# Optimization experiments

Hardware: AMD Instinct MI355X
Metric: run time of the kernel (lower is better)

The kernel has to match this reference:

```python
import jax, jax.numpy as jnp
import numpy as np

N_NODES = 200000
N_EDGES = 3200000
N_FEAT = 8
DT_INIT = 0.3
DT_MIN, DT_MAX = 0.02, 2.0
CG_MAX_ITER = 30
CG_TOL = 1e-4
G_INIT = 9.81


def setup_inputs() -> dict:
    key = jax.random.key(0)
    k1, k2, k3, k4 = jax.random.split(key, 4)
    u_now = jax.random.normal(k1, (N_NODES, N_FEAT), dtype=jnp.float32)
    # DAG edges: src < dst (required by the module's topo-level build)
    a = jax.random.randint(k2, (N_EDGES,), 0, N_NODES)
    b = jax.random.randint(k3, (N_EDGES,), 0, N_NODES)
    src = jnp.minimum(a, b)
    dst = jnp.maximum(a, b)
    dst = jnp.where(src == dst, jnp.minimum(dst + 1, N_NODES - 1), dst)
    src = jnp.where(src == dst, jnp.maximum(src - 1, 0), src)
    edge_index = jnp.stack([src, dst]).astype(jnp.int64)
    # edge_attr[:,0]=dx (positive), edge_attr[:,1]=dz
    edge_attr = jax.random.uniform(k4, (N_EDGES, 2), dtype=jnp.float32,
                                   minval=0.05, maxval=1.0)
    dt = jnp.asarray(DT_INIT, dtype=jnp.float32)
    g_hat = jnp.asarray(G_INIT, dtype=jnp.float32)
    return {"u_now": u_now, "edge_index": edge_index, "edge_attr": edge_attr,
            "dt": dt, "g_hat": g_hat}


def _cg_solve(mv, rhs, max_iter, tol):
    # matches torch cg_solve with x0=None (zeros)
    x = jnp.zeros_like(rhs)
    r = rhs - mv(x)
    p = r
    rs = jnp.sum(r * r)

    def body(i, state):
        x, r, p, rs, done = state
        Ap = mv(p)
        alpha = rs / (jnp.sum(p * Ap) + 1e-12)
        x1 = x + alpha * p
        r1 = r - alpha * Ap
        rs1 = jnp.sum(r1 * r1)
        done1 = done | (jnp.sqrt(rs1) <= tol)
        beta = rs1 / (rs + 1e-12)
        p1 = r1 + beta * p
        sel = lambda old, new: jnp.where(done, old, new)
        return (sel(x, x1), sel(r, r1), sel(p, p1),
                jnp.where(done, rs, rs1), done1)

    x, _, _, _, _ = jax.lax.fori_loop(
        0, max_iter, body, (x, r, p, rs, jnp.array(False)))
    return x


def reference(u_now, edge_index, edge_attr, dt, g_hat):
    src, dst = edge_index[0], edge_index[1]
    E = src.shape[0]
    F = u_now.shape[1]
    dx = jnp.clip(edge_attr[:, 0], 1e-6, None)        # [E]
    inv = (1.0 / dx)[:, None]                         # [E,1]
    slope_e = (edge_attr[:, 1] / dx)[:, None]         # [E,1] dz/dx
    dt_eff = jnp.clip(dt, DT_MIN, DT_MAX)

    def D1(x):  # upwind: out[i] += (x[i]-x[j])*inv_dx
        return jnp.zeros_like(x).at[dst].add((x[dst] - x[src]) * inv)

    def D1_T(y):
        yd = y[dst] * inv
        return jnp.zeros_like(y).at[dst].add(yd).at[src].add(-yd)

    A_mv = lambda v: v + dt_eff * (u_now * D1(v))
    AT_mv = lambda y: y + dt_eff * D1_T(u_now * y)

    # slope source term scattered to dst nodes
    slope_n = jnp.zeros_like(u_now).at[dst].add(
        jnp.broadcast_to(slope_e, (E, F)))
    b = u_now - dt_eff * g_hat * slope_n

    # necg: solve (A^T A) x = A^T b via CG
    rhs = AT_mv(b)
    mv = lambda v: AT_mv(A_mv(v))
    u_next = _cg_solve(mv, rhs, CG_MAX_ITER, CG_TOL)
    return u_next
```

## Files before the change

### kernel.cpp

```cpp
#include <hip/hip_runtime.h>
#include <math.h>
#include <stdint.h>
#include <string.h>


#define F 8
#define CG_ITERS 30
#define LEAF_T 4096
#define LEAF_PAD (LEAF_T + LEAF_T / 128 + 8)
#define ENC_ADD 1024
#define MAX_LEAF 1024
#define MAX_CLS 32


#define LV(A_, i_) A_[(i_) + ((i_) >> 7)]

struct Sched {
    int NL, uNT, uMaxD, nCls;
    int leafOff[MAX_LEAF], leafN[MAX_LEAF], cls[MAX_LEAF];
    int cNB[MAX_CLS], cMaxD[MAX_CLS];
    int cBOff[MAX_CLS][64], cBN[MAX_CLS][64];
    int cA[MAX_CLS][64], cB[MAX_CLS][64], cOrder[MAX_CLS][64];
    int cLevOff[MAX_CLS][32];
    int uA[MAX_LEAF], uB[MAX_LEAF], uOrder[MAX_LEAF], uLevOff[64];
};


static void host_build_tree(int n, int T, int* bOff, int* bN,
                            int* A, int* B, int* dep,
                            int* pNB, int* pNT, int* pMaxD) {
    int so[64], sn[64], st[64], sid[64], sdp[64];
    int sp = 0, coff = 0, cn = n, c2 = 0, t = 0, rootd = 0;
    for (;;) {
        if (cn <= T) {
            if (bOff) { bOff[c2] = coff; bN[c2] = cn; }
            int id = c2, dp = 0; c2++;
            bool fin = false;
            for (;;) {
                if (sp == 0) { rootd = dp; fin = true; break; }
                if (st[sp - 1] == 0) {
                    st[sp - 1] = 1; sid[sp - 1] = id; sdp[sp - 1] = dp;
                    int n2 = sn[sp - 1] / 2; n2 -= (n2 & 7);
                    coff = so[sp - 1] + n2; cn = sn[sp - 1] - n2;
                    break;
                } else {
                    A[t] = sid[sp - 1]; B[t] = id;
                    int dA = sdp[sp - 1];
                    dp = ((dA > dp) ? dA : dp) + 1;
                    dep[t] = dp;
                    id = ENC_ADD + t; t++;
                    sp--;
                }
            }
            if (fin) break;
        } else {
            so[sp] = coff; sn[sp] = cn; st[sp] = 0; sp++;
            int n2 = cn / 2; n2 -= (n2 & 7);
            cn = n2;
        }
    }
    *pNB = c2; *pNT = t; *pMaxD = rootd;
}

static void host_bucketize(const int* dep, int NT, int maxD,
                           int* order, int* levOff) {
    int cnt[64];
    for (int d = 0; d <= maxD; ++d) cnt[d] = 0;
    for (int t = 0; t < NT; ++t) cnt[dep[t]]++;
    int run = 0;
    levOff[0] = 0;
    for (int d = 1; d <= maxD; ++d) { run += cnt[d]; levOff[d] = run; }
    int cur[64];
    for (int d = 1; d <= maxD; ++d) cur[d] = levOff[d - 1];
    for (int t = 0; t < NT; ++t) { int d = dep[t]; order[cur[d]++] = t; }
}

static void build_sched_host(int n, Sched* s) {
    static int uDep[MAX_LEAF];
    host_build_tree(n, LEAF_T, s->leafOff, s->leafN, s->uA, s->uB, uDep,
                    &s->NL, &s->uNT, &s->uMaxD);
    host_bucketize(uDep, s->uNT, s->uMaxD, s->uOrder, s->uLevOff);
    s->nCls = 0;
    int clsN[MAX_CLS];
    int dep[64];
    for (int j = 0; j < s->NL; ++j) {
        int c = -1;
        for (int k = 0; k < s->nCls; ++k)
            if (clsN[k] == s->leafN[j]) { c = k; break; }
        if (c < 0 && s->nCls < MAX_CLS) {
            c = s->nCls++;
            clsN[c] = s->leafN[j];
            int NB, NT, maxD;
            host_build_tree(s->leafN[j], 128, s->cBOff[c], s->cBN[c],
                            s->cA[c], s->cB[c], dep, &NB, &NT, &maxD);
            s->cNB[c] = NB; s->cMaxD[c] = maxD;
            host_bucketize(dep, NT, maxD, s->cOrder[c], s->cLevOff[c]);
        }
        s->cls[j] = c;
    }
}


__device__ __forceinline__ float dt_eff_of(const float* dtp) {
    return fminf(fmaxf(dtp[0], 0.02f), 2.0f);
}

__device__ __forceinline__ int slotOf(int e, int NB) {
    return (e < ENC_ADD) ? e : (NB + (e - ENC_ADD));
}

__device__ __forceinline__ float combine_upper(const float* __restrict__ partial,
                                               const Sched* __restrict__ sc,
                                               float* sU, int lane) {
    int NL = sc->NL, NT = sc->uNT, maxD = sc->uMaxD;
    for (int k = lane; k < NL; k += 256) sU[k] = partial[k];
    __syncthreads();
    for (int d = 1; d <= maxD; ++d) {
        int s0 = sc->uLevOff[d - 1], s1 = sc->uLevOff[d];
        for (int s = s0 + lane; s < s1; s += 256) {
            int tt = sc->uOrder[s];
            sU[NL + tt] = __fadd_rn(sU[slotOf(sc->uA[tt], NL)],
                                    sU[slotOf(sc->uB[tt], NL)]);
        }
        __syncthreads();
    }
    return (NT > 0) ? sU[NL + NT - 1] : sU[0];
}

__device__ __forceinline__ void dot_eval(const float* sA, const float* sB,
                                         float* sChain, float* sVal,
                                         int lane, int NB,
                                         const int* __restrict__ bOff,
                                         const int* __restrict__ bN,
                                         const int* __restrict__ A,
                                         const int* __restrict__ Bb,
                                         const int* __restrict__ order,
                                         const int* __restrict__ levOff,
                                         int maxD,
                                         float* __restrict__ partial, int j) {
    int bb = lane >> 3, jj = lane & 7;
    if (bb < NB) {
        int off = bOff[bb], n = bN[bb];
        if (n >= 8) {
            int lim = n - (n & 7);
            float rr = __fmul_rn(LV(sA, off + jj), LV(sB, off + jj));
            for (int e = jj + 8; e < lim; e += 8)
                rr = __fadd_rn(rr, __fmul_rn(LV(sA, off + e), LV(sB, off + e)));
            sChain[bb * 8 + jj] = rr;
        }
    }
    __syncthreads();
    if (lane < NB) {
        int off = bOff[lane], n = bN[lane];
        float res;
        if (n < 8) {
            res = 0.f;
            for (int e = 0; e < n; ++e)
                res = __fadd_rn(res, __fmul_rn(LV(sA, off + e), LV(sB, off + e)));
        } else {
            int lim = n - (n & 7);
            const float* c = sChain + lane * 8;
            res = __fadd_rn(__fadd_rn(__fadd_rn(c[0], c[1]), __fadd_rn(c[2], c[3])),
                            __fadd_rn(__fadd_rn(c[4], c[5]), __fadd_rn(c[6], c[7])));
            for (int e = lim; e < n; ++e)
                res = __fadd_rn(res, __fmul_rn(LV(sA, off + e), LV(sB, off + e)));
        }
        sVal[lane] = res;
    }
    __syncthreads();
    for (int d = 1; d <= maxD; ++d) {
        int s0 = levOff[d - 1], s1 = levOff[d];
        for (int s = s0 + lane; s < s1; s += 256) {
            int tt = order[s];
            sVal[NB + tt] = __fadd_rn(sVal[slotOf(A[tt], NB)],
                                      sVal[slotOf(Bb[tt], NB)]);
        }
        __syncthreads();
    }
    if (lane == 0) partial[j] = (NB > 1) ? sVal[NB + NB - 2] : sVal[0];
}

__global__ void k_dot_leaf(const float* __restrict__ a, const float* __restrict__ b,
                           const Sched* __restrict__ sc, float* __restrict__ partial) {
    __shared__ float sA[LEAF_PAD], sB[LEAF_PAD];
    __shared__ float sChain[512];
    __shared__ float sVal[160];
    int j = blockIdx.x, lane = threadIdx.x;
    int P = sc->leafOff[j] + 1, nn = sc->leafN[j];
    for (int g = lane; g < nn; g += 256) {
        float av = a[P + g], bv = b[P + g];
        int m = g + (g >> 7);
        sA[m] = av; sB[m] = bv;
    }
    __syncthreads();
    int c = sc->cls[j];
    dot_eval(sA, sB, sChain, sVal, lane, sc->cNB[c], sc->cBOff[c], sc->cBN[c],
             sc->cA[c], sc->cB[c], sc->cOrder[c], sc->cLevOff[c], sc->cMaxD[c],
             partial, j);
}

__global__ void k_dot_rs0(const float* __restrict__ a,
                          const float* __restrict__ partial,
                          const Sched* __restrict__ sc, float* __restrict__ scal) {
    __shared__ float sU[2048];
    int lane = threadIdx.x;
    float res = combine_upper(partial, sc, sU, lane);
    if (lane == 0)
        scal[8 + 0] = __fadd_rn(__fmul_rn(a[0], a[0]), res);
}

__global__ void k_xr_dot(float* __restrict__ x, float* __restrict__ r,
                         const float* __restrict__ p, const float* __restrict__ z,
                         const float* __restrict__ scal,
                         const Sched* __restrict__ sc,
                         const float* __restrict__ partial1,
                         float* __restrict__ partial2, int it) {
    __shared__ float sA[LEAF_PAD];
    __shared__ float sU[2048];
    __shared__ float sChain[512];
    __shared__ float sVal[160];
    __shared__ float sAl;
    __shared__ int   sAct;
    int j = blockIdx.x, lane = threadIdx.x;
    float res = combine_upper(partial1, sc, sU, lane);
    if (lane == 0) {
        float pt = __fadd_rn(__fmul_rn(p[0], z[0]), res);
        sAl = __fdiv_rn(scal[8 + it], __fadd_rn(pt, (float)1e-12));
        sAct = (scal[64 + it] == 0.f) ? 1 : 0;
    }
    __syncthreads();
    int active = sAct;
    float al = sAl;
    int P = sc->leafOff[j] + 1, nn = sc->leafN[j];
    if (j == 0 && lane == 0 && active) {
        x[0] = __fadd_rn(x[0], __fmul_rn(al, p[0]));
        r[0] = __fsub_rn(r[0], __fmul_rn(al, z[0]));
    }
    for (int g = lane; g < nn; g += 256) {
        int q = P + g;
        float rv = r[q];
        if (active) {
            float xv = x[q], pv = p[q], zv = z[q];
            x[q] = __fadd_rn(xv, __fmul_rn(al, pv));
            rv = __fsub_rn(rv, __fmul_rn(al, zv));
            r[q] = rv;
        }
        sA[g + (g >> 7)] = rv;
    }
    __syncthreads();
    int c = sc->cls[j];
    dot_eval(sA, sA, sChain, sVal, lane, sc->cNB[c], sc->cBOff[c], sc->cBN[c],
             sc->cA[c], sc->cB[c], sc->cOrder[c], sc->cLevOff[c], sc->cMaxD[c],
             partial2, j);
}

__global__ void k_p_fin(float4* __restrict__ p4, const float4* __restrict__ r4,
                        const float* __restrict__ rfull,
                        float* __restrict__ scal,
                        const Sched* __restrict__ sc,
                        const float* __restrict__ partial2, int it, int n4) {
    __shared__ float sU[2048];
    __shared__ float sBe;
    __shared__ int   sAct;
    int lane = threadIdx.x;
    float res = combine_upper(partial2, sc, sU, lane);
    if (lane == 0) {
        float rs1 = __fadd_rn(__fmul_rn(rfull[0], rfull[0]), res);
        float RS = scal[8 + it];
        float dn = scal[64 + it];
        sBe = __fdiv_rn(rs1, __fadd_rn(RS, (float)1e-12));
        sAct = (dn == 0.f) ? 1 : 0;
        if (blockIdx.x == 0) {
            scal[8 + it + 1]  = (dn == 0.f) ? rs1 : RS;
            scal[64 + it + 1] = (dn != 0.f || __fsqrt_rn(rs1) <= (float)1e-4)
                                ? 1.f : 0.f;
        }
    }
    __syncthreads();
    if (!sAct) return;
    float be = sBe;
    int i = blockIdx.x * blockDim.x + lane;
    if (i >= n4) return;
    float4 pv = p4[i], rv = r4[i];
    pv.x = __fadd_rn(rv.x, __fmul_rn(be, pv.x));
    pv.y = __fadd_rn(rv.y, __fmul_rn(be, pv.y));
    pv.z = __fadd_rn(rv.z, __fmul_rn(be, pv.z));
    pv.w = __fadd_rn(rv.w, __fmul_rn(be, pv.w));
    p4[i] = pv;
}


__global__ void k_edge_pre(const int* __restrict__ dst, const int* __restrict__ src,
                           int* __restrict__ dstCnt, int* __restrict__ srcCnt, int E) {
    int e = blockIdx.x * blockDim.x + threadIdx.x;
    if (e >= E) return;
    atomicAdd(&dstCnt[dst[e]], 1);
    atomicAdd(&srcCnt[src[e]], 1);
}

__global__ void k_scan1(const int* __restrict__ cnt, int* __restrict__ incl,
                        int* __restrict__ bsums, int N) {
    __shared__ int sm[512];
    int i = blockIdx.x * 512 + threadIdx.x;
    sm[threadIdx.x] = (i < N) ? cnt[i] : 0;
    __syncthreads();
    for (int off = 1; off < 512; off <<= 1) {
        int t = (threadIdx.x >= off) ? sm[threadIdx.x - off] : 0;
        __syncthreads();
        sm[threadIdx.x] += t;
        __syncthreads();
    }
    if (i < N) incl[i] = sm[threadIdx.x];
    if (threadIdx.x == 511) bsums[blockIdx.x] = sm[511];
}

__global__ void k_scan2(int* __restrict__ bsums, int nb) {
    __shared__ int sm[512];
    sm[threadIdx.x] = (threadIdx.x < nb) ? bsums[threadIdx.x] : 0;
    __syncthreads();
    for (int off = 1; off < 512; off <<= 1) {
        int t = (threadIdx.x >= off) ? sm[threadIdx.x - off] : 0;
        __syncthreads();
        sm[threadIdx.x] += t;
        __syncthreads();
    }
    if (threadIdx.x < nb) bsums[threadIdx.x] = sm[threadIdx.x];
}

__global__ void k_scan3(int* __restrict__ off, const int* __restrict__ bsums,
                        const int* __restrict__ cnt, int N, int E) {
    int i = blockIdx.x * 512 + threadIdx.x;
    if (i < N) {
        int add = (blockIdx.x > 0) ? bsums[blockIdx.x - 1] : 0;
        off[i] = off[i] + add - cnt[i];
    }
    if (i == 0) off[N] = E;
}

__global__ void k_fill(const int* __restrict__ dst, const int* __restrict__ src,
                       const int* __restrict__ dstOff, const int* __restrict__ srcOff,
                       int* __restrict__ cursD, int* __restrict__ cursS,
                       int* __restrict__ dstList, int* __restrict__ srcList, int E) {
    int e = blockIdx.x * blockDim.x + threadIdx.x;
    if (e >= E) return;
    int d = dst[e];
    dstList[dstOff[d] + atomicAdd(&cursD[d], 1)] = e;
    int s0 = src[e];
    srcList[srcOff[s0] + atomicAdd(&cursS[s0], 1)] = e;
}

__device__ __forceinline__ void insort(int* L, int lo, int hi) {
    for (int a = lo + 1; a < hi; ++a) {
        int key = L[a]; int b = a - 1;
        while (b >= lo && L[b] > key) { L[b + 1] = L[b]; b--; }
        L[b + 1] = key;
    }
}

__global__ void k_sort(const int* __restrict__ dstOff, const int* __restrict__ srcOff,
                       int* __restrict__ dstList, int* __restrict__ srcList, int N) {
    int i = blockIdx.x * blockDim.x + threadIdx.x;
    if (i >= N) return;
    insort(dstList, dstOff[i], dstOff[i + 1]);
    insort(srcList, srcOff[i], srcOff[i + 1]);
}

__global__ void k_perm(int* dstList, int* srcList,
                       const int* __restrict__ srcp, const int* __restrict__ dstp,
                       const float* __restrict__ ea,
                       float* __restrict__ invD, float* __restrict__ slopeD,
                       float* __restrict__ invS, int E) {
    int k = blockIdx.x * blockDim.x + threadIdx.x;
    if (k >= E) return;
    int e  = dstList[k];
    int e2 = srcList[k];
    float dx  = fmaxf(ea[2 * e], 1e-6f);
    float dx2 = fmaxf(ea[2 * e2], 1e-6f);
    int sA_ = srcp[e];
    int dB_ = dstp[e2];
    float iD = __fdiv_rn(1.f, dx);
    float sD = __fdiv_rn(ea[2 * e + 1], dx);
    float iS = __fdiv_rn(1.f, dx2);
    dstList[k] = sA_;
    srcList[k] = dB_;
    invD[k] = iD; slopeD[k] = sD; invS[k] = iS;
}


__global__ void k_slope_b(const float* __restrict__ u, const float* __restrict__ slopeD,
                          const int* __restrict__ dstOff,
                          float* __restrict__ r, float* __restrict__ y,
                          const float* __restrict__ dtp, const float* __restrict__ gp,
                          int N) {
    int i = blockIdx.x * blockDim.x + threadIdx.x;
    if (i >= N) return;
    float dtg = __fmul_rn(dt_eff_of(dtp), gp[0]);
    float sn = 0.f;
    int k0 = dstOff[i], k1 = dstOff[i + 1];
    for (int k = k0; k < k1; ++k) sn = __fadd_rn(sn, slopeD[k]);
    float ms = __fmul_rn(dtg, sn);
    const float4* u4 = (const float4*)u;
    float4* r4 = (float4*)r;
    float4* y4 = (float4*)y;
    #pragma unroll
    for (int hh = 0; hh < 2; ++hh) {
        float4 uv = u4[i * 2 + hh];
        float4 bv;
        bv.x = __fsub_rn(uv.x, ms);
        bv.y = __fsub_rn(uv.y, ms);
        bv.z = __fsub_rn(uv.z, ms);
        bv.w = __fsub_rn(uv.w, ms);
        r4[i * 2 + hh] = bv;
        float4 yv;
        yv.x = __fmul_rn(uv.x, bv.x);
        yv.y = __fmul_rn(uv.y, bv.y);
        yv.z = __fmul_rn(uv.z, bv.z);
        yv.w = __fmul_rn(uv.w, bv.w);
        y4[i * 2 + hh] = yv;
    }
}

__global__ void k_d1tz(const int* __restrict__ dstB, const int* __restrict__ dstOff,
                       const float* __restrict__ invD, const int* __restrict__ srcOff,
                       const float* __restrict__ invS, const float* __restrict__ y,
                       const float* __restrict__ base, float* __restrict__ out,
                       const float* __restrict__ dtp,
                       float* __restrict__ rInit, float* __restrict__ xInit,
                       int doInit, int NP) {
    int idx = blockIdx.x * blockDim.x + threadIdx.x;
    if (idx >= NP) return;
    int i = idx >> 2, c = idx & 3;
    const float2* y2 = (const float2*)y;
    float2 uy = y2[idx];
    float2 acc = make_float2(0.f, 0.f);
    int k0 = dstOff[i], k1 = dstOff[i + 1];
    #pragma unroll 4
    for (int k = k0; k < k1; ++k) {
        float iv = invD[k];
        acc.x = __fadd_rn(acc.x, __fmul_rn(uy.x, iv));
        acc.y = __fadd_rn(acc.y, __fmul_rn(uy.y, iv));
    }
    k0 = srcOff[i]; k1 = srcOff[i + 1];
    #pragma unroll 4
    for (int k = k0; k < k1; ++k) {
        int d = dstB[k];
        float iv = invS[k];
        float2 yd = y2[d * 4 + c];
        float t0 = __fmul_rn(yd.x, iv); acc.x = __fadd_rn(acc.x, -t0);
        float t1 = __fmul_rn(yd.y, iv); acc.y = __fadd_rn(acc.y, -t1);
    }
    float dt = dt_eff_of(dtp);
    float2 bs = ((const float2*)base)[idx];
    float2 ov;
    ov.x = __fadd_rn(bs.x, __fmul_rn(dt, acc.x));
    ov.y = __fadd_rn(bs.y, __fmul_rn(dt, acc.y));
    ((float2*)out)[idx] = ov;
    if (doInit) {
        ((float2*)rInit)[idx] = ov;
        ((float2*)xInit)[idx] = make_float2(0.f, 0.f);
    }
}

__global__ void k_d1w(const int* __restrict__ srcA, const int* __restrict__ dstOff,
                      const float* __restrict__ invD, const float* __restrict__ pv,
                      const float* __restrict__ u,
                      float* __restrict__ w, float* __restrict__ y,
                      const float* __restrict__ dtp, int NP) {
    int idx = blockIdx.x * blockDim.x + threadIdx.x;
    if (idx >= NP) return;
    int i = idx >> 2, c = idx & 3;
    const float2* pv2 = (const float2*)pv;
    float2 pi = pv2[idx];
    float2 acc = make_float2(0.f, 0.f);
    int k0 = dstOff[i], k1 = dstOff[i + 1];
    #pragma unroll 4
    for (int k = k0; k < k1; ++k) {
        int s = srcA[k];
        float iv = invD[k];
        float2 ps = pv2[s * 4 + c];
        acc.x = __fadd_rn(acc.x, __fmul_rn(__fsub_rn(pi.x, ps.x), iv));
        acc.y = __fadd_rn(acc.y, __fmul_rn(__fsub_rn(pi.y, ps.y), iv));
    }
    float dt = dt_eff_of(dtp);
    float2 uv = ((const float2*)u)[idx];
    float2 wv;
    wv.x = __fadd_rn(pi.x, __fmul_rn(dt, __fmul_rn(uv.x, acc.x)));
    wv.y = __fadd_rn(pi.y, __fmul_rn(dt, __fmul_rn(uv.y, acc.y)));
    ((float2*)w)[idx] = wv;
    float2 yv;
    yv.x = __fmul_rn(uv.x, wv.x);
    yv.y = __fmul_rn(uv.y, wv.y);
    ((float2*)y)[idx] = yv;
}

extern "C" void kernel_launch(void* const* d_in, const int* in_sizes, int n_in,
                              void* d_out, int out_size, void* d_ws, size_t ws_size,
                              hipStream_t stream) {
    const float* u   = (const float*)d_in[0];
    const int*   ei  = (const int*)d_in[1];
    const float* ea  = (const float*)d_in[2];
    const float* dtp = (const float*)d_in[3];
    const float* gp  = (const float*)d_in[4];

    const int NF = in_sizes[0];
    const int N  = NF / F;
    const int E  = in_sizes[2] / 2;
    const int* srcp = ei;
    const int* dstp = ei + E;

    static Sched h_sched;
    build_sched_host(NF - 1, &h_sched);
    const int NL = h_sched.NL;

    char* wp = (char*)d_ws;
    float* scal    = (float*)wp; wp += 128 * 4;
    float* r       = (float*)wp; wp += (size_t)NF * 4;
    float* p       = (float*)wp; wp += (size_t)NF * 4;
    float* t       = (float*)wp; wp += (size_t)NF * 4;
    float* w       = (float*)wp; wp += (size_t)NF * 4;
    float* y       = (float*)wp; wp += (size_t)NF * 4;
    int*   dstList = (int*)wp;   wp += (size_t)E * 4;
    int*   srcList = (int*)wp;   wp += (size_t)E * 4;
    float* invD    = (float*)wp; wp += (size_t)E * 4;
    float* invS    = (float*)wp; wp += (size_t)E * 4;
    float* slopeD  = (float*)wp; wp += (size_t)E * 4;
    int*   dstOff  = (int*)wp;   wp += (size_t)(N + 1) * 4;
    int*   srcOff  = (int*)wp;   wp += (size_t)(N + 1) * 4;
    int*   dstCnt  = (int*)wp;   wp += (size_t)N * 4;
    int*   srcCnt  = (int*)wp;   wp += (size_t)N * 4;
    int*   cursD   = (int*)wp;   wp += (size_t)N * 4;
    int*   cursS   = (int*)wp;   wp += (size_t)N * 4;
    int*   bsD     = (int*)wp;   wp += 512 * 4;
    int*   bsS     = (int*)wp;   wp += 512 * 4;
    float* partial1 = (float*)wp; wp += 2048 * 4;
    float* partial2 = (float*)wp; wp += 2048 * 4;
    wp = (char*)(((uintptr_t)wp + 255) & ~(uintptr_t)255);
    Sched* d_sched = (Sched*)wp; wp += (sizeof(Sched) + 255) & ~(size_t)255;
    float* x = (float*)d_out;

    hipMemcpyAsync(d_sched, &h_sched, sizeof(Sched), hipMemcpyHostToDevice,
                   stream);
    hipMemsetAsync(scal, 0, 128 * 4, stream);
    hipMemsetAsync(dstCnt, 0, (size_t)N * 4, stream);
    hipMemsetAsync(srcCnt, 0, (size_t)N * 4, stream);
    hipMemsetAsync(cursD, 0, (size_t)N * 4, stream);
    hipMemsetAsync(cursS, 0, (size_t)N * 4, stream);

    const int bn = 256;
    const int gN  = (N + bn - 1) / bn;
    const int gE  = (E + bn - 1) / bn;
    const int nb  = (N + 511) / 512;
    const int n4  = NF / 4;
    const int g4  = (n4 + bn - 1) / bn;
    const int NP  = NF / 2;
    const int gP  = (NP + bn - 1) / bn;

    k_edge_pre<<<gE, bn, 0, stream>>>(dstp, srcp, dstCnt, srcCnt, E);
    k_scan1<<<nb, 512, 0, stream>>>(dstCnt, dstOff, bsD, N);
    k_scan2<<<1, 512, 0, stream>>>(bsD, nb);
    k_scan3<<<nb, 512, 0, stream>>>(dstOff, bsD, dstCnt, N, E);
    k_scan1<<<nb, 512, 0, stream>>>(srcCnt, srcOff, bsS, N);
    k_scan2<<<1, 512, 0, stream>>>(bsS, nb);
    k_scan3<<<nb, 512, 0, stream>>>(srcOff, bsS, srcCnt, N, E);
    k_fill<<<gE, bn, 0, stream>>>(dstp, srcp, dstOff, srcOff, cursD, cursS,
                                  dstList, srcList, E);
    k_sort<<<gN, bn, 0, stream>>>(dstOff, srcOff, dstList, srcList, N);
    k_perm<<<gE, bn, 0, stream>>>(dstList, srcList, srcp, dstp, ea,
                                  invD, slopeD, invS, E);
    const int* srcA = dstList;
    const int* dstB = srcList;

    k_slope_b<<<gN, bn, 0, stream>>>(u, slopeD, dstOff, r, y, dtp, gp, N);
    k_d1tz<<<gP, bn, 0, stream>>>(dstB, dstOff, invD, srcOff, invS,
                                  y, r, p, dtp, r, x, 1, NP);
    k_dot_leaf<<<NL, 256, 0, stream>>>(p, p, d_sched, partial1);
    k_dot_rs0<<<1, 256, 0, stream>>>(p, partial1, d_sched, scal);

    for (int it = 0; it < CG_ITERS; ++it) {
        k_d1w<<<gP, bn, 0, stream>>>(srcA, dstOff, invD, p, u, w, y, dtp, NP);
        k_d1tz<<<gP, bn, 0, stream>>>(dstB, dstOff, invD, srcOff, invS,
                                      y, w, t, dtp, (float*)0, (float*)0, 0, NP);
        k_dot_leaf<<<NL, 256, 0, stream>>>(p, t, d_sched, partial1);
        k_xr_dot<<<NL, 256, 0, stream>>>(x, r, p, t, scal, d_sched,
                                         partial1, partial2, it);
        k_p_fin<<<g4, bn, 0, stream>>>((float4*)p, (const float4*)r, r, scal,
                                       d_sched, partial2, it, n4);
    }
}
```

Before: 5.033 ms.

## Pack edge index and inverse-dx into AoS and move dst-side D1T sum into d1w

Edge neighbor indices and 1/dx weights are interleaved into one 8-byte struct per edge for both the dst-sorted and src-sorted CSR lists, so each gather loop does one vector load instead of two separate streams. The dst-side term of D1^T (y_i times the sum of inv over incoming edges) is now computed in the D1 kernel right after y is produced and stored in a new dacc buffer, so the transpose kernel only walks the src list. Splitting the loop this way adds an extra NF-sized buffer write and read per iteration, but it avoids re-walking the dst list in the second kernel and reuses edD while it is still warm in cache.

Result: faster. 4.812 ms (-4.4%).

```diff
diff --git a/kernel.cpp b/kernel.cpp
--- a/kernel.cpp
+++ b/kernel.cpp
@@ -14,6 +14,8 @@
 
 
 #define LV(A_, i_) A_[(i_) + ((i_) >> 7)]
+
+struct __align__(8) Ed { int n; float v; };
 
 struct Sched {
     int NL, uNT, uMaxD, nCls;
@@ -365,25 +367,23 @@
     insort(srcList, srcOff[i], srcOff[i + 1]);
 }
 
-__global__ void k_perm(int* dstList, int* srcList,
+__global__ void k_perm(const int* __restrict__ dstList, const int* __restrict__ srcList,
                        const int* __restrict__ srcp, const int* __restrict__ dstp,
                        const float* __restrict__ ea,
-                       float* __restrict__ invD, float* __restrict__ slopeD,
-                       float* __restrict__ invS, int E) {
+                       Ed* __restrict__ edD, float* __restrict__ slopeD,
+                       Ed* __restrict__ edS, int E) {
     int k = blockIdx.x * blockDim.x + threadIdx.x;
     if (k >= E) return;
     int e  = dstList[k];
     int e2 = srcList[k];
     float dx  = fmaxf(ea[2 * e], 1e-6f);
     float dx2 = fmaxf(ea[2 * e2], 1e-6f);
-    int sA_ = srcp[e];
-    int dB_ = dstp[e2];
-    float iD = __fdiv_rn(1.f, dx);
+    Ed d0; d0.n = srcp[e];  d0.v = __fdiv_rn(1.f, dx);
+    Ed s0; s0.n = dstp[e2]; s0.v = __fdiv_rn(1.f, dx2);
     float sD = __fdiv_rn(ea[2 * e + 1], dx);
-    float iS = __fdiv_rn(1.f, dx2);
-    dstList[k] = sA_;
-    srcList[k] = dB_;
-    invD[k] = iD; slopeD[k] = sD; invS[k] = iS;
+    edD[k] = d0;
+    edS[k] = s0;
+    slopeD[k] = sD;
 }
 
 
@@ -420,13 +420,13 @@
     }
 }
 
-__global__ void k_d1tz(const int* __restrict__ dstB, const int* __restrict__ dstOff,
-                       const float* __restrict__ invD, const int* __restrict__ srcOff,
-                       const float* __restrict__ invS, const float* __restrict__ y,
-                       const float* __restrict__ base, float* __restrict__ out,
-                       const float* __restrict__ dtp,
-                       float* __restrict__ rInit, float* __restrict__ xInit,
-                       int doInit, int NP) {
+__global__ void k_d1tz_full(const Ed* __restrict__ edD, const int* __restrict__ dstOff,
+                            const Ed* __restrict__ edS, const int* __restrict__ srcOff,
+                            const float* __restrict__ y,
+                            const float* __restrict__ base, float* __restrict__ out,
+                            const float* __restrict__ dtp,
+                            float* __restrict__ rInit, float* __restrict__ xInit,
+                            int NP) {
     int idx = blockIdx.x * blockDim.x + threadIdx.x;
     if (idx >= NP) return;
     int i = idx >> 2, c = idx & 3;
@@ -436,18 +436,17 @@
     int k0 = dstOff[i], k1 = dstOff[i + 1];
     #pragma unroll 4
     for (int k = k0; k < k1; ++k) {
-        float iv = invD[k];
+        float iv = edD[k].v;
         acc.x = __fadd_rn(acc.x, __fmul_rn(uy.x, iv));
         acc.y = __fadd_rn(acc.y, __fmul_rn(uy.y, iv));
     }
     k0 = srcOff[i]; k1 = srcOff[i + 1];
     #pragma unroll 4
     for (int k = k0; k < k1; ++k) {
-        int d = dstB[k];
-        float iv = invS[k];
-        float2 yd = y2[d * 4 + c];
-        float t0 = __fmul_rn(yd.x, iv); acc.x = __fadd_rn(acc.x, -t0);
-        float t1 = __fmul_rn(yd.y, iv); acc.y = __fadd_rn(acc.y, -t1);
+        Ed e = edS[k];
+        float2 yd = y2[e.n * 4 + c];
+        float t0 = __fmul_rn(yd.x, e.v); acc.x = __fadd_rn(acc.x, -t0);
+        float t1 = __fmul_rn(yd.y, e.v); acc.y = __fadd_rn(acc.y, -t1);
     }
     float dt = dt_eff_of(dtp);
     float2 bs = ((const float2*)base)[idx];
@@ -455,17 +454,15 @@
     ov.x = __fadd_rn(bs.x, __fmul_rn(dt, acc.x));
     ov.y = __fadd_rn(bs.y, __fmul_rn(dt, acc.y));
     ((float2*)out)[idx] = ov;
-    if (doInit) {
-        ((float2*)rInit)[idx] = ov;
-        ((float2*)xInit)[idx] = make_float2(0.f, 0.f);
-    }
-}
-
-__global__ void k_d1w(const int* __restrict__ srcA, const int* __restrict__ dstOff,
-                      const float* __restrict__ invD, const float* __restrict__ pv,
-                      const float* __restrict__ u,
-                      float* __restrict__ w, float* __restrict__ y,
-                      const float* __restrict__ dtp, int NP) {
+    ((float2*)rInit)[idx] = ov;
+    ((float2*)xInit)[idx] = make_float2(0.f, 0.f);
+}
+
+__global__ void k_d1w_f(const Ed* __restrict__ edD, const int* __restrict__ dstOff,
+                        const float* __restrict__ pv, const float* __restrict__ u,
+                        float* __restrict__ w, float* __restrict__ y,
+                        float* __restrict__ dacc,
+                        const float* __restrict__ dtp, int NP) {
     int idx = blockIdx.x * blockDim.x + threadIdx.x;
     if (idx >= NP) return;
     int i = idx >> 2, c = idx & 3;
@@ -475,11 +472,10 @@
     int k0 = dstOff[i], k1 = dstOff[i + 1];
     #pragma unroll 4
     for (int k = k0; k < k1; ++k) {
-        int s = srcA[k];
-        float iv = invD[k];
-        float2 ps = pv2[s * 4 + c];
-        acc.x = __fadd_rn(acc.x, __fmul_rn(__fsub_rn(pi.x, ps.x), iv));
-        acc.y = __fadd_rn(acc.y, __fmul_rn(__fsub_rn(pi.y, ps.y), iv));
+        Ed e = edD[k];
+        float2 ps = pv2[e.n * 4 + c];
+        acc.x = __fadd_rn(acc.x, __fmul_rn(__fsub_rn(pi.x, ps.x), e.v));
+        acc.y = __fadd_rn(acc.y, __fmul_rn(__fsub_rn(pi.y, ps.y), e.v));
     }
     float dt = dt_eff_of(dtp);
     float2 uv = ((const float2*)u)[idx];
@@ -491,6 +487,39 @@
     yv.x = __fmul_rn(uv.x, wv.x);
     yv.y = __fmul_rn(uv.y, wv.y);
     ((float2*)y)[idx] = yv;
+    float2 da = make_float2(0.f, 0.f);
+    #pragma unroll 4
+    for (int k = k0; k < k1; ++k) {
+        float iv = edD[k].v;
+        da.x = __fadd_rn(da.x, __fmul_rn(yv.x, iv));
+        da.y = __fadd_rn(da.y, __fmul_rn(yv.y, iv));
+    }
+    ((float2*)dacc)[idx] = da;
+}
+
+__global__ void k_d1tzs(const Ed* __restrict__ edS, const int* __restrict__ srcOff,
+                        const float* __restrict__ y, const float* __restrict__ dacc,
+                        const float* __restrict__ base, float* __restrict__ out,
+                        const float* __restrict__ dtp, int NP) {
+    int idx = blockIdx.x * blockDim.x + threadIdx.x;
+    if (idx >= NP) return;
+    int i = idx >> 2, c = idx & 3;
+    const float2* y2 = (const float2*)y;
+    float2 acc = ((const float2*)dacc)[idx];
+    int k0 = srcOff[i], k1 = srcOff[i + 1];
+    #pragma unroll 4
+    for (int k = k0; k < k1; ++k) {
+        Ed e = edS[k];
+        float2 yd = y2[e.n * 4 + c];
+        float t0 = __fmul_rn(yd.x, e.v); acc.x = __fadd_rn(acc.x, -t0);
+        float t1 = __fmul_rn(yd.y, e.v); acc.y = __fadd_rn(acc.y, -t1);
+    }
+    float dt = dt_eff_of(dtp);
+    float2 bs = ((const float2*)base)[idx];
+    float2 ov;
+    ov.x = __fadd_rn(bs.x, __fmul_rn(dt, acc.x));
+    ov.y = __fadd_rn(bs.y, __fmul_rn(dt, acc.y));
+    ((float2*)out)[idx] = ov;
 }
 
 extern "C" void kernel_launch(void* const* d_in, const int* in_sizes, int n_in,
@@ -519,10 +548,11 @@
     float* t       = (float*)wp; wp += (size_t)NF * 4;
     float* w       = (float*)wp; wp += (size_t)NF * 4;
     float* y       = (float*)wp; wp += (size_t)NF * 4;
+    float* dacc    = (float*)wp; wp += (size_t)NF * 4;
     int*   dstList = (int*)wp;   wp += (size_t)E * 4;
     int*   srcList = (int*)wp;   wp += (size_t)E * 4;
-    float* invD    = (float*)wp; wp += (size_t)E * 4;
-    float* invS    = (float*)wp; wp += (size_t)E * 4;
+    Ed*    edD     = (Ed*)wp;    wp += (size_t)E * 8;
+    Ed*    edS     = (Ed*)wp;    wp += (size_t)E * 8;
     float* slopeD  = (float*)wp; wp += (size_t)E * 4;
     int*   dstOff  = (int*)wp;   wp += (size_t)(N + 1) * 4;
     int*   srcOff  = (int*)wp;   wp += (size_t)(N + 1) * 4;
@@ -566,20 +596,17 @@
                                   dstList, srcList, E);
     k_sort<<<gN, bn, 0, stream>>>(dstOff, srcOff, dstList, srcList, N);
     k_perm<<<gE, bn, 0, stream>>>(dstList, srcList, srcp, dstp, ea,
-                                  invD, slopeD, invS, E);
-    const int* srcA = dstList;
-    const int* dstB = srcList;
+                                  edD, slopeD, edS, E);
 
     k_slope_b<<<gN, bn, 0, stream>>>(u, slopeD, dstOff, r, y, dtp, gp, N);
-    k_d1tz<<<gP, bn, 0, stream>>>(dstB, dstOff, invD, srcOff, invS,
-                                  y, r, p, dtp, r, x, 1, NP);
+    k_d1tz_full<<<gP, bn, 0, stream>>>(edD, dstOff, edS, srcOff,
+                                       y, r, p, dtp, r, x, NP);
     k_dot_leaf<<<NL, 256, 0, stream>>>(p, p, d_sched, partial1);
     k_dot_rs0<<<1, 256, 0, stream>>>(p, partial1, d_sched, scal);
 
     for (int it = 0; it < CG_ITERS; ++it) {
-        k_d1w<<<gP, bn, 0, stream>>>(srcA, dstOff, invD, p, u, w, y, dtp, NP);
-        k_d1tz<<<gP, bn, 0, stream>>>(dstB, dstOff, invD, srcOff, invS,
-                                      y, w, t, dtp, (float*)0, (float*)0, 0, NP);
+        k_d1w_f<<<gP, bn, 0, stream>>>(edD, dstOff, p, u, w, y, dacc, dtp, NP);
+        k_d1tzs<<<gP, bn, 0, stream>>>(edS, srcOff, y, dacc, w, t, dtp, NP);
         k_dot_leaf<<<NL, 256, 0, stream>>>(p, t, d_sched, partial1);
         k_xr_dot<<<NL, 256, 0, stream>>>(x, r, p, t, scal, d_sched,
                                          partial1, partial2, it);
```
